# Optimization experiments

Measured on AMD Instinct MI355X. Metric: run time of the kernel, lower is better.

The kernel has to match this reference:

```python
import jax, jax.numpy as jnp
import numpy as np

SEQ_LEN = 65536
HIDDEN = 1024

def setup_inputs() -> dict:
    key = jax.random.key(0)
    k1, k2 = jax.random.split(key)
    hidden = jax.random.normal(k1, (HIDDEN,), dtype=jnp.float32)
    encoder_outputs = jax.random.normal(k2, (SEQ_LEN, HIDDEN), dtype=jnp.float32)
    return {"hidden": hidden, "encoder_outputs": encoder_outputs}

def reference(hidden, encoder_outputs):
    # method == 'dot': energies[i] = hidden . encoder_outputs[i]
    # vectorized: one matvec [S,H]@[H] -> [S]
    energies = jnp.einsum('sh,h->s', encoder_outputs, hidden)
    attn = jax.nn.softmax(energies, axis=-1)
    return attn[None, None, :]  # [1, 1, S] as in original unsqueeze(0).unsqueeze(0)
```

## Files before the change

kernel.cpp:

```cpp
#include <hip/hip_runtime.h>

#define SEQ 65536
#define HID 1024
#define K1_BLOCKS 2048
#define WPB 4
#define NWAVES (K1_BLOCKS * WPB)
#define RPW (SEQ / NWAVES)

typedef float f4 __attribute__((ext_vector_type(4)));

__global__ __launch_bounds__(256) void k_matvec_stats(
        const float* __restrict__ enc,
        const float* __restrict__ hid,
        float* __restrict__ energies,
        float2* __restrict__ stats) {
    const int lane = threadIdx.x & 63;
    const int wid  = threadIdx.x >> 6;
    const int gw   = blockIdx.x * WPB + wid;
    const size_t base = (size_t)gw * RPW;

    const f4* __restrict__ h4 = (const f4*)hid;
    const f4 h0 = h4[lane];
    const f4 h1 = h4[lane + 64];
    const f4 h2 = h4[lane + 128];
    const f4 h3 = h4[lane + 192];

    float wmax = -INFINITY, wsum = 0.0f;
    #pragma unroll
    for (int r = 0; r < RPW; ++r) {
        const f4* __restrict__ row = (const f4*)(enc + (base + r) * HID);
        f4 a0 = __builtin_nontemporal_load(row + lane);
        f4 a1 = __builtin_nontemporal_load(row + lane + 64);
        f4 a2 = __builtin_nontemporal_load(row + lane + 128);
        f4 a3 = __builtin_nontemporal_load(row + lane + 192);
        float s = a0.x*h0.x + a0.y*h0.y + a0.z*h0.z + a0.w*h0.w
                + a1.x*h1.x + a1.y*h1.y + a1.z*h1.z + a1.w*h1.w
                + a2.x*h2.x + a2.y*h2.y + a2.z*h2.z + a2.w*h2.w
                + a3.x*h3.x + a3.y*h3.y + a3.z*h3.z + a3.w*h3.w;
        #pragma unroll
        for (int off = 32; off >= 1; off >>= 1)
            s += __shfl_xor(s, off, 64);
        if (lane == 0) energies[base + r] = s;
        float nm = fmaxf(wmax, s);
        wsum = wsum * __expf(wmax - nm) + __expf(s - nm);
        wmax = nm;
    }

    __shared__ float sm[WPB], ss[WPB];
    if (lane == 0) { sm[wid] = wmax; ss[wid] = wsum; }
    __syncthreads();
    if (threadIdx.x == 0) {
        float m = fmaxf(fmaxf(sm[0], sm[1]), fmaxf(sm[2], sm[3]));
        float s = ss[0]*__expf(sm[0]-m) + ss[1]*__expf(sm[1]-m)
                + ss[2]*__expf(sm[2]-m) + ss[3]*__expf(sm[3]-m);
        stats[blockIdx.x] = make_float2(m, s);
    }
}

__global__ __launch_bounds__(256) void k_softmax_scale(
        float* __restrict__ out,
        const float2* __restrict__ stats) {
    float m = -INFINITY, s = 0.0f;
    #pragma unroll
    for (int k = 0; k < K1_BLOCKS / 256; ++k) {
        float2 st = stats[k * 256 + threadIdx.x];
        float nm = fmaxf(m, st.x);
        s = s * __expf(m - nm) + st.y * __expf(st.x - nm);
        m = nm;
    }
    #pragma unroll
    for (int off = 32; off >= 1; off >>= 1) {
        float om = __shfl_xor(m, off, 64);
        float os = __shfl_xor(s, off, 64);
        float nm = fmaxf(m, om);
        s = s * __expf(m - nm) + os * __expf(om - nm);
        m = nm;
    }
    __shared__ float sm[4], ss[4];
    const int lane = threadIdx.x & 63, wid = threadIdx.x >> 6;
    if (lane == 0) { sm[wid] = m; ss[wid] = s; }
    __syncthreads();
    const float M = fmaxf(fmaxf(sm[0], sm[1]), fmaxf(sm[2], sm[3]));
    const float S = ss[0]*__expf(sm[0]-M) + ss[1]*__expf(sm[1]-M)
                  + ss[2]*__expf(sm[2]-M) + ss[3]*__expf(sm[3]-M);
    const float invS = 1.0f / S;

    const int i = (blockIdx.x * 256 + threadIdx.x) * 4;
    float4 e = *(const float4*)(out + i);
    e.x = __expf(e.x - M) * invS;
    e.y = __expf(e.y - M) * invS;
    e.z = __expf(e.z - M) * invS;
    e.w = __expf(e.w - M) * invS;
    *(float4*)(out + i) = e;
}

extern "C" void kernel_launch(void* const* d_in, const int* in_sizes, int n_in,
                              void* d_out, int out_size, void* d_ws, size_t ws_size,
                              hipStream_t stream) {
    const float* hid = (const float*)d_in[0];
    const float* enc = (const float*)d_in[1];
    float* out = (float*)d_out;
    float2* stats = (float2*)d_ws;

    k_matvec_stats  <<<K1_BLOCKS, 256, 0, stream>>>(enc, hid, out, stats);
    k_softmax_scale <<<SEQ / (256 * 4), 256, 0, stream>>>(out, stats);
}
```

Baseline: 48.24 us.

## Fuse matvec and softmax scaling into one cooperative kernel with grid sync

Merges the matvec and stats kernel with the normalization kernel into a single cooperative launch that uses a grid-wide sync between phases. The grid shrinks from 2048 to 1024 blocks so every block can be co-resident, which doubles the rows per wave, and the row loop is only partially unrolled. The goal is to drop the second kernel launch and its launch gap. In exchange it pays for a grid barrier and has fewer waves in flight to hide memory latency during the bandwidth-bound matvec.

```diff
diff --git a/kernel.cpp b/kernel.cpp
--- a/kernel.cpp
+++ b/kernel.cpp
@@ -1,18 +1,22 @@
 #include <hip/hip_runtime.h>
+#include <hip/hip_cooperative_groups.h>
+
+namespace cg = cooperative_groups;
 
 #define SEQ 65536
 #define HID 1024
-#define K1_BLOCKS 2048
+#define BLOCKS 1024
 #define WPB 4
-#define NWAVES (K1_BLOCKS * WPB)
-#define RPW (SEQ / NWAVES)
+#define NW (BLOCKS * WPB)
+#define RPW (SEQ / NW)
+#define CHUNK (SEQ / BLOCKS)
 
 typedef float f4 __attribute__((ext_vector_type(4)));
 
-__global__ __launch_bounds__(256) void k_matvec_stats(
+__global__ __launch_bounds__(256, 4) void k_fused(
         const float* __restrict__ enc,
         const float* __restrict__ hid,
-        float* __restrict__ energies,
+        float* __restrict__ out,
         float2* __restrict__ stats) {
     const int lane = threadIdx.x & 63;
     const int wid  = threadIdx.x >> 6;
@@ -26,7 +30,7 @@
     const f4 h3 = h4[lane + 192];
 
     float wmax = -INFINITY, wsum = 0.0f;
-    #pragma unroll
+    #pragma unroll 4
     for (int r = 0; r < RPW; ++r) {
         const f4* __restrict__ row = (const f4*)(enc + (base + r) * HID);
         f4 a0 = __builtin_nontemporal_load(row + lane);
@@ -40,7 +44,7 @@
         #pragma unroll
         for (int off = 32; off >= 1; off >>= 1)
             s += __shfl_xor(s, off, 64);
-        if (lane == 0) energies[base + r] = s;
+        if (lane == 0) out[base + r] = s;
         float nm = fmaxf(wmax, s);
         wsum = wsum * __expf(wmax - nm) + __expf(s - nm);
         wmax = nm;
@@ -55,14 +59,12 @@
                 + ss[2]*__expf(sm[2]-m) + ss[3]*__expf(sm[3]-m);
         stats[blockIdx.x] = make_float2(m, s);
     }
-}
 
-__global__ __launch_bounds__(256) void k_softmax_scale(
-        float* __restrict__ out,
-        const float2* __restrict__ stats) {
+    cg::this_grid().sync();
+
     float m = -INFINITY, s = 0.0f;
     #pragma unroll
-    for (int k = 0; k < K1_BLOCKS / 256; ++k) {
+    for (int k = 0; k < BLOCKS / 256; ++k) {
         float2 st = stats[k * 256 + threadIdx.x];
         float nm = fmaxf(m, st.x);
         s = s * __expf(m - nm) + st.y * __expf(st.x - nm);
@@ -76,22 +78,23 @@
         s = s * __expf(m - nm) + os * __expf(om - nm);
         m = nm;
     }
-    __shared__ float sm[4], ss[4];
-    const int lane = threadIdx.x & 63, wid = threadIdx.x >> 6;
-    if (lane == 0) { sm[wid] = m; ss[wid] = s; }
+    __shared__ float sm2[WPB], ss2[WPB];
+    if (lane == 0) { sm2[wid] = m; ss2[wid] = s; }
     __syncthreads();
-    const float M = fmaxf(fmaxf(sm[0], sm[1]), fmaxf(sm[2], sm[3]));
-    const float S = ss[0]*__expf(sm[0]-M) + ss[1]*__expf(sm[1]-M)
-                  + ss[2]*__expf(sm[2]-M) + ss[3]*__expf(sm[3]-M);
+    const float M = fmaxf(fmaxf(sm2[0], sm2[1]), fmaxf(sm2[2], sm2[3]));
+    const float S = ss2[0]*__expf(sm2[0]-M) + ss2[1]*__expf(sm2[1]-M)
+                  + ss2[2]*__expf(sm2[2]-M) + ss2[3]*__expf(sm2[3]-M);
     const float invS = 1.0f / S;
 
-    const int i = (blockIdx.x * 256 + threadIdx.x) * 4;
-    float4 e = *(const float4*)(out + i);
-    e.x = __expf(e.x - M) * invS;
-    e.y = __expf(e.y - M) * invS;
-    e.z = __expf(e.z - M) * invS;
-    e.w = __expf(e.w - M) * invS;
-    *(float4*)(out + i) = e;
+    if (threadIdx.x < CHUNK / 4) {
+        const int i = blockIdx.x * CHUNK + threadIdx.x * 4;
+        float4 e = *(const float4*)(out + i);
+        e.x = __expf(e.x - M) * invS;
+        e.y = __expf(e.y - M) * invS;
+        e.z = __expf(e.z - M) * invS;
+        e.w = __expf(e.w - M) * invS;
+        *(float4*)(out + i) = e;
+    }
 }
 
 extern "C" void kernel_launch(void* const* d_in, const int* in_sizes, int n_in,
@@ -102,6 +105,7 @@
     float* out = (float*)d_out;
     float2* stats = (float2*)d_ws;
 
-    k_matvec_stats  <<<K1_BLOCKS, 256, 0, stream>>>(enc, hid, out, stats);
-    k_softmax_scale <<<SEQ / (256 * 4), 256, 0, stream>>>(out, stats);
+    void* args[] = { (void*)&enc, (void*)&hid, (void*)&out, (void*)&stats };
+    hipLaunchCooperativeKernel((const void*)k_fused,
+                               dim3(BLOCKS), dim3(256), args, 0, stream);
 }
```

Result: slower. 170.8 us (+254.0%).
